# Kernel optimization log

Hardware: AMD Instinct MI355X
Metric: run time of the kernel (lower is better)

The kernel has to match this reference:

```python
import jax, jax.numpy as jnp
import numpy as np

BATCH, HORIZON = 512, 512
DIM_IN, DIM_OUT, DIM_X, DIM_NL = 64, 64, 256, 128
EPS = 1e-3  # pos_def_tol
STD = 0.5   # initialization_std


def setup_inputs() -> dict:
    key = jax.random.key(0)
    ks = jax.random.split(key, 7)
    n2 = 2 * DIM_X + DIM_NL  # 640
    return {
        "u_in": jax.random.normal(ks[0], (BATCH, HORIZON, DIM_IN), jnp.float32),
        "X":   jax.random.normal(ks[1], (n2, n2), jnp.float32) * STD,
        "Y":   jax.random.normal(ks[2], (DIM_X, DIM_X), jnp.float32) * STD,
        "B2":  jax.random.normal(ks[3], (DIM_X, DIM_IN), jnp.float32) * STD,
        "C2":  jax.random.normal(ks[4], (DIM_OUT, DIM_X), jnp.float32) * STD,
        "D21": jax.random.normal(ks[5], (DIM_OUT, DIM_NL), jnp.float32) * STD,
        "D12": jax.random.normal(ks[6], (DIM_NL, DIM_IN), jnp.float32) * STD,
    }


def _ren_run(u_in, X, Y, B2, C2, D21, D12):
    n, q = DIM_X, DIM_NL
    # Contraction-preserving matrix construction: H = X^T X + eps*I, block split.
    H = X.T @ X + EPS * jnp.eye(2 * n + q, dtype=X.dtype)
    H11 = H[:n, :n]
    H21 = H[n:n + q, :n]
    H22 = H[n:n + q, n:n + q]
    H31 = H[n + q:, :n]
    H32 = H[n + q:, n:n + q]
    H33 = H[n + q:, n + q:]
    Fm, B1 = H31, H32
    E = 0.5 * (H11 + H33 + Y - Y.T)
    E_inv = jnp.linalg.inv(E)
    Lam = 0.5 * jnp.diag(H22)          # (q,) positive diagonal of Lambda
    D11 = -jnp.tril(H22, -1)           # strictly lower triangular
    C1 = -H21

    batch, horizon = u_in.shape[0], u_in.shape[1]
    x0 = jnp.zeros((batch, n), u_in.dtype)  # x_init = 0 (defaults)

    def step(x, u_t):
        # Terms not depending on w (hoisted out of the substitution loop).
        base = x @ C1.T + u_t @ D12.T  # (B, q)

        # Forward substitution through the implicit layer: w_i = tanh(v_i / Lam_i),
        # with v_i depending only on w_{<i} since D11 is strictly lower triangular.
        def body(i, w):
            v = base[:, i] + w @ D11[i]          # (B,)
            return w.at[:, i].set(jnp.tanh(v / Lam[i]))

        w = jax.lax.fori_loop(0, q, body, jnp.zeros((batch, q), u_in.dtype))
        x_new = (x @ Fm.T + w @ B1.T + u_t @ B2.T) @ E_inv.T
        y = x_new @ C2.T + w @ D21.T
        return x_new, y

    # run(): first output is y_init (= C2 @ x_init = 0), then horizon-1 forward steps.
    u_seq = jnp.swapaxes(u_in[:, :horizon - 1, :], 0, 1)  # (T-1, B, dim_in)
    _, ys = jax.lax.scan(step, x0, u_seq)                 # (T-1, B, dim_out)
    y0 = jnp.zeros((batch, 1, DIM_OUT), u_in.dtype)
    return jnp.concatenate([y0, jnp.swapaxes(ys, 0, 1)], axis=1)


def reference(u_in, X, Y, B2, C2, D21, D12):
    return _ren_run(u_in, X, Y, B2, C2, D21, D12)
```

## Files before the change

### kernel.cpp

```cpp
#include <hip/hip_runtime.h>
#include <math.h>
#include <stddef.h>

#define NTWO 640
#define DXN 256
#define DNLN 128
#define DINN 64
#define DOUTN 64
#define BATCHN 512
#define HORN 512
#define EPSV 1.0e-3

typedef unsigned int uint;
typedef unsigned short ushort;
typedef _Float16 half2_t __attribute__((ext_vector_type(2)));

__device__ __forceinline__ float fdot2(uint a, uint b, float c) {
#if __has_builtin(__builtin_amdgcn_fdot2)
  return __builtin_amdgcn_fdot2(__builtin_bit_cast(half2_t, a),
                                __builtin_bit_cast(half2_t, b), c, false);
#else
  half2_t x = __builtin_bit_cast(half2_t, a), y = __builtin_bit_cast(half2_t, b);
  return c + (float)x[0] * (float)y[0] + (float)x[1] * (float)y[1];
#endif
}

__device__ __forceinline__ uint pack_f16(float x, float y) {
  _Float16 hx = (_Float16)x, hy = (_Float16)y;
  ushort ux = __builtin_bit_cast(ushort, hx), uy = __builtin_bit_cast(ushort, hy);
  return ((uint)uy << 16) | (uint)ux;
}

__device__ __forceinline__ float fast_exp2(float x) {
#if __has_builtin(__builtin_amdgcn_exp2f)
  return __builtin_amdgcn_exp2f(x);
#else
  return exp2f(x);
#endif
}

__device__ __forceinline__ float bcast_lane(float v, int l) {
#if __has_builtin(__builtin_amdgcn_readlane)
  return __builtin_bit_cast(float, __builtin_amdgcn_readlane(__builtin_bit_cast(int, v), l));
#else
  return __shfl(v, l, 64);
#endif
}

__device__ __forceinline__ uint comp4(const uint4& v, int k) {
  switch (k & 3) {
    case 0: return v.x;
    case 1: return v.y;
    case 2: return v.z;
    default: return v.w;
  }
}


__global__ void k_xtx(const float* __restrict__ X, double* __restrict__ H) {
  __shared__ float sA[16][17];
  __shared__ float sB[16][17];
  const int tx = threadIdx.x, ty = threadIdx.y;
  const int bi = blockIdx.y * 16, bj = blockIdx.x * 16;
  double acc = 0.0;
  for (int k0 = 0; k0 < NTWO; k0 += 16) {
    sA[ty][tx] = X[(k0 + ty) * NTWO + bi + tx];
    sB[ty][tx] = X[(k0 + ty) * NTWO + bj + tx];
    __syncthreads();
#pragma unroll
    for (int kk = 0; kk < 16; ++kk)
      acc += (double)sA[kk][ty] * (double)sB[kk][tx];
    __syncthreads();
  }
  const int i = bi + ty, j = bj + tx;
  if (i == j) acc += EPSV;
  H[i * NTWO + j] = acc;
}

__global__ void k_prep(const double* __restrict__ H, const float* __restrict__ Y,
                       const float* __restrict__ B2, const float* __restrict__ C2,
                       const float* __restrict__ D21,
                       double* __restrict__ E, double* __restrict__ scv,
                       double* __restrict__ B2d, double* __restrict__ C2d,
                       double* __restrict__ Dxt, double* __restrict__ Eye2) {
  int idx = blockIdx.x * 256 + threadIdx.x;
  if (idx < 65536) {
    int i = idx >> 8, j = idx & 255;
    E[idx] = 0.5 * (H[i * NTWO + j] + H[(384 + i) * NTWO + 384 + j]
                    + (double)Y[i * 256 + j] - (double)Y[j * 256 + i]);
    return;
  }
  idx -= 65536;
  if (idx < 128) {
    double lam = 0.5 * H[(256 + idx) * NTWO + 256 + idx];
    scv[idx] = 2.8853900817779268 / lam;
    return;
  }
  idx -= 128;
  if (idx < 16384) { B2d[idx] = (double)B2[idx]; return; }
  idx -= 16384;
  if (idx < 16384) { C2d[idx] = (double)C2[idx]; return; }
  idx -= 16384;
  if (idx < 28672) {
    int r = idx / 448, c = idx % 448;
    double v = 0.0;
    if (c >= 256 && c < 384) v = (double)D21[r * 128 + (c - 256)];
    Dxt[idx] = v;
    return;
  }
  idx -= 28672;
  if (idx < 16384) {
    int r = idx >> 7, c = idx & 127;
    Eye2[idx] = (r == c) ? 2.0 : 0.0;
  }
}

__global__ void k_ginv32(const double* __restrict__ A, int lda, float* __restrict__ Out) {
  __shared__ float M[128 * 129];
  const int tid = threadIdx.x;
  for (int i = tid; i < 128 * 128; i += 256)
    M[(i >> 7) * 129 + (i & 127)] = (float)A[(i >> 7) * lda + (i & 127)];
  __syncthreads();
  for (int k = 0; k < 128; ++k) {
    float ip = 1.0f / M[k * 129 + k];
    __syncthreads();
    if (tid < 128) {
      float v = M[k * 129 + tid];
      M[k * 129 + tid] = (tid == k) ? ip : v * ip;
    }
    __syncthreads();
    const int i0 = tid >> 1, half = tid & 1;
    float f = (i0 != k) ? M[i0 * 129 + k] : 0.0f;
    __syncthreads();
    if (i0 != k) {
      const float* rk = M + k * 129;
      float* ri = M + i0 * 129;
      const int j0 = half * 64;
#pragma unroll 8
      for (int j = j0; j < j0 + 64; ++j) {
        float v = (j == k) ? 0.0f : ri[j];
        ri[j] = v - f * rk[j];
      }
    }
    __syncthreads();
  }
  for (int i = tid; i < 128 * 128; i += 256) Out[i] = M[(i >> 7) * 129 + (i & 127)];
}

__global__ void k_dgemm(int M, int N, int K,
                        const double* __restrict__ A, int lda,
                        const double* __restrict__ B, int ldb,
                        double alpha,
                        const double* __restrict__ D, int ldd, double beta,
                        double* __restrict__ C, int ldc) {
  __shared__ double sA[16][17];
  __shared__ double sB[16][17];
  const int tx = threadIdx.x, ty = threadIdx.y;
  const int row = blockIdx.y * 16 + ty, col = blockIdx.x * 16 + tx;
  double acc = 0.0;
  for (int k0 = 0; k0 < K; k0 += 16) {
    sA[ty][tx] = A[row * lda + k0 + tx];
    sB[ty][tx] = B[(k0 + ty) * ldb + col];
    __syncthreads();
#pragma unroll
    for (int kk = 0; kk < 16; ++kk) acc += sA[ty][kk] * sB[kk][tx];
    __syncthreads();
  }
  double v = alpha * acc;
  if (beta != 0.0) v += beta * D[row * ldd + col];
  C[row * ldc + col] = v;
}

__global__ void k_copyblk(const double* __restrict__ S, int lds,
                          double* __restrict__ Dst, int ldd, int total, int cols) {
  int idx = blockIdx.x * 256 + threadIdx.x;
  if (idx < total) {
    int r = idx / cols, c = idx % cols;
    Dst[r * ldd + c] = S[r * lds + c];
  }
}

__global__ void k_cast_f2d(const float* __restrict__ s, double* __restrict__ d, int n) {
  int i = blockIdx.x * 256 + threadIdx.x;
  if (i < n) d[i] = (double)s[i];
}

__global__ void k_pack(const double* __restrict__ H, const float* __restrict__ D12,
                       const double* __restrict__ sc, const double* __restrict__ Axwu,
                       const double* __restrict__ G,
                       uint* __restrict__ Msh, uint* __restrict__ OmWh,
                       uint* __restrict__ Tp1g, uint* __restrict__ Tp2g) {
  int idx = blockIdx.x * 256 + threadIdx.x;
  if (idx < 448 * 160) {
    int rr = idx / 160, d = idx % 160;
    float v[2];
#pragma unroll
    for (int e = 0; e < 2; ++e) {
      int k = 2 * d + e;
      double x;
      if (rr < 128) {
        double s = sc[rr];
        x = (k < 256) ? (-H[(256 + rr) * NTWO + k] * s)
                      : ((double)D12[rr * DINN + (k - 256)] * s);
      } else {
        int r2 = rr - 128;
        const double* src = (r2 < 256) ? (Axwu + (size_t)r2 * 448) : (G + (size_t)(r2 - 256) * 448);
        x = (k < 256) ? src[k] : src[384 + (k - 256)];
      }
      v[e] = (float)x;
    }
    Msh[((size_t)(d >> 2) * 448 + rr) * 4 + (d & 3)] = pack_f16(v[0], v[1]);
    return;
  }
  idx -= 448 * 160;
  if (idx < 320 * 64) {
    int rr = idx / 64, d = idx % 64;
    float v[2];
#pragma unroll
    for (int e = 0; e < 2; ++e) {
      int j = 2 * d + e;
      double x = (rr < 256) ? Axwu[(size_t)rr * 448 + 256 + j]
                            : G[(size_t)(rr - 256) * 448 + 256 + j];
      v[e] = (float)x;
    }
    OmWh[((size_t)(d >> 2) * 320 + rr) * 4 + (d & 3)] = pack_f16(v[0], v[1]);
    return;
  }
  idx -= 320 * 64;
  if (idx < 4096) {
    int l = idx >> 6, d = idx & 63;
    float lo = (l > d) ? (float)(-H[(256 + l) * NTWO + 256 + d] * sc[l]) : 0.0f;
    float hi = (float)(-H[(256 + l + 64) * NTWO + 256 + d] * sc[l + 64]);
    Tp1g[idx] = pack_f16(lo, hi);
    return;
  }
  idx -= 4096;
  if (idx < 2048) {
    int l = idx >> 5, i = idx & 31;
    int j0 = 64 + 2 * i, j1 = j0 + 1;
    float v0 = (l + 64 > j0) ? (float)(-H[(256 + l + 64) * NTWO + 256 + j0] * sc[l + 64]) : 0.0f;
    float v1 = (l + 64 > j1) ? (float)(-H[(256 + l + 64) * NTWO + 256 + j1] * sc[l + 64]) : 0.0f;
    Tp2g[idx] = pack_f16(v0, v1);
  }
}

__global__ __launch_bounds__(512)
void k_scan(const float* __restrict__ u_in, const uint* __restrict__ Msh,
            const uint* __restrict__ OmWh, const uint* __restrict__ Tp1g,
            const uint* __restrict__ Tp2g, float* __restrict__ out) {
  __shared__ uint4 baseL4[40 * 128];
  __shared__ uint Tp1L[64 * 68];
  __shared__ uint Tp2L[64 * 36];
  __shared__ uint __align__(16) zL[2 * 164];
  __shared__ uint __align__(16) wvhL[2 * 64];
  const int tid = threadIdx.x;
  const int s0 = blockIdx.x * 2;
  const uint4* __restrict__ mp4 = (const uint4*)Msh;
  const uint4* __restrict__ op4 = (const uint4*)OmWh;

  for (int i = tid; i < 5120; i += 512) {
    const int blk = i >> 7, r = i & 127;
    baseL4[i] = mp4[(size_t)blk * 448 + r];
  }
  for (int i = tid; i < 4096; i += 512) Tp1L[(i >> 6) * 68 + (i & 63)] = Tp1g[i];
  for (int i = tid; i < 2048; i += 512) Tp2L[(i >> 5) * 36 + (i & 31)] = Tp2g[i];
  if (tid < 256) zL[(tid >> 7) * 164 + (tid & 127)] = 0u;
  if (tid < 128) out[((size_t)(s0 + (tid >> 6)) * HORN) * DOUTN + (tid & 63)] = 0.0f;
  if (tid >= 448) {
    const int i = tid - 448, s = i >> 5, k = i & 31;
    const float* up = u_in + ((size_t)(s0 + s) * HORN) * DINN + 2 * k;
    zL[s * 164 + 128 + k] = pack_f16(up[0], up[1]);
  }
  __syncthreads();

  for (int t = 0; t < HORN - 1; ++t) {
    float a0 = 0.f, a1 = 0.f;
    float unx = 0.f, uny = 0.f;
    uint4 om[16];
    if (tid < 128) {
      const int b = tid >> 6, l = tid & 63;
      uint4 q[16], r2[8];
      {
        const uint* tp1 = Tp1L + l * 68;
        const uint* tp2 = Tp2L + l * 36;
#pragma unroll
        for (int i = 0; i < 16; ++i) q[i] = *(const uint4*)(tp1 + 4 * i);
#pragma unroll
        for (int i = 0; i < 8; ++i) r2[i] = *(const uint4*)(tp2 + 4 * i);
      }
      const uint4* zz = (const uint4*)(zL + b * 164);
      float c0 = 0.f, c1 = 0.f;
#pragma unroll 8
      for (int i = 0; i < 40; ++i) {
        const uint4 mA = baseL4[i * 128 + l];
        const uint4 mB = baseL4[i * 128 + 64 + l];
        const uint4 p = zz[i];
        c0 = fdot2(mA.x, p.x, c0); c0 = fdot2(mA.y, p.y, c0);
        c0 = fdot2(mA.z, p.z, c0); c0 = fdot2(mA.w, p.w, c0);
        c1 = fdot2(mB.x, p.x, c1); c1 = fdot2(mB.y, p.y, c1);
        c1 = fdot2(mB.z, p.z, c1); c1 = fdot2(mB.w, p.w, c1);
      }
      __builtin_amdgcn_s_setprio(1);
      float wx = 0.f, wy = 0.f;
#pragma unroll
      for (int j = 0; j < 64; ++j) {
        const float av = bcast_lane(c0, j);
        const float sx = fast_exp2(av);
        const float rc = __builtin_amdgcn_rcpf(sx + 1.0f);
        const float w = __builtin_fmaf(-2.0f, rc, 1.0f);
        if (l == (j >> 1)) { if (j & 1) wy = w; else wx = w; }
        const half2_t h = __builtin_bit_cast(half2_t, comp4(q[j >> 2], j & 3));
        c0 = __builtin_fmaf((float)h[0], w, c0);
        c1 = __builtin_fmaf((float)h[1], w, c1);
      }
#pragma unroll
      for (int j = 64; j < 128; ++j) {
        const float av = bcast_lane(c1, j - 64);
        const float sx = fast_exp2(av);
        const float rc = __builtin_amdgcn_rcpf(sx + 1.0f);
        const float w = __builtin_fmaf(-2.0f, rc, 1.0f);
        if (l == (j >> 1)) { if (j & 1) wy = w; else wx = w; }
        const int i2 = j - 64;
        const half2_t h = __builtin_bit_cast(half2_t, comp4(r2[i2 >> 3], (i2 >> 1) & 3));
        const float tv = (i2 & 1) ? (float)h[1] : (float)h[0];
        c1 = __builtin_fmaf(tv, w, c1);
      }
      __builtin_amdgcn_s_setprio(0);
      wvhL[b * 64 + l] = pack_f16(wx, wy);
    } else if (tid < 448) {
      const int row = tid;
      const uint4* z0 = (const uint4*)zL;
      const uint4* z1 = (const uint4*)(zL + 164);
      uint4 mbuf[20];
#pragma unroll
      for (int i = 0; i < 20; ++i) mbuf[i] = mp4[(size_t)i * 448 + row];
#pragma unroll
      for (int i = 0; i < 20; ++i) {
        const uint4 m = mbuf[i];
        const uint4 p = z0[i], q = z1[i];
        a0 = fdot2(m.x, p.x, a0); a0 = fdot2(m.y, p.y, a0);
        a0 = fdot2(m.z, p.z, a0); a0 = fdot2(m.w, p.w, a0);
        a1 = fdot2(m.x, q.x, a1); a1 = fdot2(m.y, q.y, a1);
        a1 = fdot2(m.z, q.z, a1); a1 = fdot2(m.w, q.w, a1);
      }
#pragma unroll
      for (int i = 0; i < 20; ++i) mbuf[i] = mp4[(size_t)(20 + i) * 448 + row];
#pragma unroll
      for (int i = 0; i < 20; ++i) {
        const uint4 m = mbuf[i];
        const uint4 p = z0[20 + i], q = z1[20 + i];
        a0 = fdot2(m.x, p.x, a0); a0 = fdot2(m.y, p.y, a0);
        a0 = fdot2(m.z, p.z, a0); a0 = fdot2(m.w, p.w, a0);
        a1 = fdot2(m.x, q.x, a1); a1 = fdot2(m.y, q.y, a1);
        a1 = fdot2(m.z, q.z, a1); a1 = fdot2(m.w, q.w, a1);
      }
      const int rr = row - 128;
#pragma unroll
      for (int i = 0; i < 16; ++i) om[i] = op4[(size_t)i * 320 + rr];
    } else {
      const int i = tid - 448, s = i >> 5, k = i & 31;
      const float* up = u_in + ((size_t)(s0 + s) * HORN + (t + 1)) * DINN + 2 * k;
      unx = up[0]; uny = up[1];
    }
    __syncthreads();

    if (tid >= 128 && tid < 448) {
      const int row = tid;
      const uint4* wp0 = (const uint4*)wvhL;
      const uint4* wp1 = (const uint4*)(wvhL + 64);
#pragma unroll
      for (int i = 0; i < 16; ++i) {
        const uint4 m = om[i];
        const uint4 p = wp0[i], q = wp1[i];
        a0 = fdot2(m.x, p.x, a0); a0 = fdot2(m.y, p.y, a0);
        a0 = fdot2(m.z, p.z, a0); a0 = fdot2(m.w, p.w, a0);
        a1 = fdot2(m.x, q.x, a1); a1 = fdot2(m.y, q.y, a1);
        a1 = fdot2(m.z, q.z, a1); a1 = fdot2(m.w, q.w, a1);
      }
      if (row < 384) {
        const float n0 = __shfl_down(a0, 1, 64);
        const float n1 = __shfl_down(a1, 1, 64);
        if ((row & 1) == 0) {
          const int d = (row - 128) >> 1;
          zL[d] = pack_f16(a0, n0);
          zL[164 + d] = pack_f16(a1, n1);
        }
      } else {
        const int yr = row - 384;
        out[((size_t)s0 * HORN + (t + 1)) * DOUTN + yr] = a0;
        out[((size_t)(s0 + 1) * HORN + (t + 1)) * DOUTN + yr] = a1;
      }
    } else if (tid >= 448) {
      const int i = tid - 448, s = i >> 5, k = i & 31;
      zL[s * 164 + 128 + k] = pack_f16(unx, uny);
    }
    __syncthreads();
  }
}

extern "C" void kernel_launch(void* const* d_in, const int* in_sizes, int n_in,
                              void* d_out, int out_size, void* d_ws, size_t ws_size,
                              hipStream_t stream) {
  (void)in_sizes; (void)n_in; (void)out_size; (void)ws_size;
  const float* u_in = (const float*)d_in[0];
  const float* X    = (const float*)d_in[1];
  const float* Y    = (const float*)d_in[2];
  const float* B2   = (const float*)d_in[3];
  const float* C2   = (const float*)d_in[4];
  const float* D21  = (const float*)d_in[5];
  const float* D12  = (const float*)d_in[6];
  float* out = (float*)d_out;

  double* H    = (double*)d_ws;
  double* E    = H + 640 * 640;
  double* Ai   = E + 256 * 256;
  double* CMm  = Ai + 128 * 128;
  double* MBm  = CMm + 128 * 128;
  double* Sm   = MBm + 128 * 128;
  double* Tm   = Sm + 128 * 128;
  double* Einv = Tm + 128 * 128;
  double* Axwu = Einv + 256 * 256;
  double* G    = Axwu + 256 * 448;
  double* B2d  = G + 64 * 448;
  double* C2d  = B2d + 256 * 64;
  double* Dxt  = C2d + 64 * 256;
  double* Eye2 = Dxt + 64 * 448;
  double* M0d  = Eye2 + 128 * 128;
  double* Rb   = M0d + 128 * 128;
  double* scv  = Rb + 128 * 128;
  float*  F32  = (float*)(scv + 128);
  uint*   Msh  = (uint*)(F32 + 128 * 128);
  uint*   OmWh = Msh + 71680;
  uint*   Tp1g = OmWh + 20480;
  uint*   Tp2g = Tp1g + 4096;

  dim3 blk16(16, 16);
  k_xtx<<<dim3(40, 40), blk16, 0, stream>>>(X, H);
  k_prep<<<561, 256, 0, stream>>>(H, Y, B2, C2, D21, E, scv, B2d, C2d, Dxt, Eye2);

  auto inv128 = [&](const double* A, int lda, double* Out) {
    k_ginv32<<<1, 256, 0, stream>>>(A, lda, F32);
    k_cast_f2d<<<64, 256, 0, stream>>>(F32, M0d, 128 * 128);
    k_dgemm<<<dim3(8, 8), blk16, 0, stream>>>(128, 128, 128, A, lda, M0d, 128, -1.0, Eye2, 128, 1.0, Rb, 128);
    k_dgemm<<<dim3(8, 8), blk16, 0, stream>>>(128, 128, 128, M0d, 128, Rb, 128, 1.0, (const double*)nullptr, 0, 0.0, Out, 128);
  };

  const double* EA = E;
  const double* EB = E + 128;
  const double* EC = E + 128 * 256;
  const double* ED = E + 128 * 256 + 128;

  inv128(EA, 256, Ai);
  k_dgemm<<<dim3(8, 8), blk16, 0, stream>>>(128, 128, 128, EC, 256, Ai, 128, 1.0, (const double*)nullptr, 0, 0.0, CMm, 128);
  k_dgemm<<<dim3(8, 8), blk16, 0, stream>>>(128, 128, 128, Ai, 128, EB, 256, 1.0, (const double*)nullptr, 0, 0.0, MBm, 128);
  k_dgemm<<<dim3(8, 8), blk16, 0, stream>>>(128, 128, 128, CMm, 128, EB, 256, -1.0, ED, 256, 1.0, Sm, 128);
  inv128(Sm, 128, Tm);
  k_dgemm<<<dim3(8, 8), blk16, 0, stream>>>(128, 128, 128, Tm, 128, CMm, 128, -1.0, (const double*)nullptr, 0, 0.0, Einv + 128 * 256, 256);
  k_dgemm<<<dim3(8, 8), blk16, 0, stream>>>(128, 128, 128, MBm, 128, Tm, 128, -1.0, (const double*)nullptr, 0, 0.0, Einv + 128, 256);
  k_dgemm<<<dim3(8, 8), blk16, 0, stream>>>(128, 128, 128, MBm, 128, Einv + 128 * 256, 256, -1.0, Ai, 128, 1.0, Einv, 256);
  k_copyblk<<<64, 256, 0, stream>>>(Tm, 128, Einv + 128 * 256 + 128, 256, 128 * 128, 128);

  k_dgemm<<<dim3(24, 16), blk16, 0, stream>>>(256, 384, 256, Einv, 256, H + 384 * NTWO, NTWO, 1.0, (const double*)nullptr, 0, 0.0, Axwu, 448);
  k_dgemm<<<dim3(4, 16), blk16, 0, stream>>>(256, 64, 256, Einv, 256, B2d, 64, 1.0, (const double*)nullptr, 0, 0.0, Axwu + 384, 448);
  k_dgemm<<<dim3(28, 4), blk16, 0, stream>>>(64, 448, 256, C2d, 256, Axwu, 448, 1.0, Dxt, 448, 1.0, G, 448);

  k_pack<<<384, 256, 0, stream>>>(H, D12, scv, Axwu, G, Msh, OmWh, Tp1g, Tp2g);

  k_scan<<<BATCHN / 2, 512, 0, stream>>>(u_in, Msh, OmWh, Tp1g, Tp2g, out);
}
```

Measured before the change: 4.250 ms.

## Solve nonlinearity substitution two elements at a time using tanh addition identity

Rewrites the serial forward-substitution loop so each step resolves an even/odd pair of implicit-layer outputs. The odd element is computed from the even one with the tanh addition formula (tanh(a+b) = (tanh a + tanh b)/(1 + tanh a tanh b)), using a precomputed scaled coupling coefficient. Updates then use packed half2 dot products instead of two scalar FMAs. The goal is to halve the length of the serial dependency chain and the number of cross-lane broadcasts. The cost is an extra reciprocal per pair and packed fp16 rounding (round-toward-zero conversion), which may add error.

Result: slower. 4.504 ms (+6.0%).

```diff
diff --git a/kernel.cpp b/kernel.cpp
--- a/kernel.cpp
+++ b/kernel.cpp
@@ -29,6 +29,14 @@
   _Float16 hx = (_Float16)x, hy = (_Float16)y;
   ushort ux = __builtin_bit_cast(ushort, hx), uy = __builtin_bit_cast(ushort, hy);
   return ((uint)uy << 16) | (uint)ux;
+}
+
+__device__ __forceinline__ uint pack2(float x, float y) {
+#if __has_builtin(__builtin_amdgcn_cvt_pkrtz)
+  return __builtin_bit_cast(uint, __builtin_amdgcn_cvt_pkrtz(x, y));
+#else
+  return pack_f16(x, y);
+#endif
 }
 
 __device__ __forceinline__ float fast_exp2(float x) {
@@ -189,7 +197,8 @@
                        const double* __restrict__ sc, const double* __restrict__ Axwu,
                        const double* __restrict__ G,
                        uint* __restrict__ Msh, uint* __restrict__ OmWh,
-                       uint* __restrict__ Tp1g, uint* __restrict__ Tp2g) {
+                       uint* __restrict__ TAg, uint* __restrict__ TBg,
+                       uint* __restrict__ TCg, float* __restrict__ Ts2g) {
   int idx = blockIdx.x * 256 + threadIdx.x;
   if (idx < 448 * 160) {
     int rr = idx / 160, d = idx % 160;
@@ -227,30 +236,49 @@
     return;
   }
   idx -= 320 * 64;
-  if (idx < 4096) {
-    int l = idx >> 6, d = idx & 63;
-    float lo = (l > d) ? (float)(-H[(256 + l) * NTWO + 256 + d] * sc[l]) : 0.0f;
-    float hi = (float)(-H[(256 + l + 64) * NTWO + 256 + d] * sc[l + 64]);
-    Tp1g[idx] = pack_f16(lo, hi);
-    return;
-  }
-  idx -= 4096;
   if (idx < 2048) {
-    int l = idx >> 5, i = idx & 31;
-    int j0 = 64 + 2 * i, j1 = j0 + 1;
-    float v0 = (l + 64 > j0) ? (float)(-H[(256 + l + 64) * NTWO + 256 + j0] * sc[l + 64]) : 0.0f;
-    float v1 = (l + 64 > j1) ? (float)(-H[(256 + l + 64) * NTWO + 256 + j1] * sc[l + 64]) : 0.0f;
-    Tp2g[idx] = pack_f16(v0, v1);
+    int l = idx >> 5, k = idx & 31;
+    int j0 = 2 * k, j1 = 2 * k + 1;
+    float v0 = (l > j0) ? (float)(-H[(256 + l) * NTWO + 256 + j0] * sc[l]) : 0.0f;
+    float v1 = (l > j1) ? (float)(-H[(256 + l) * NTWO + 256 + j1] * sc[l]) : 0.0f;
+    TAg[idx] = pack_f16(v0, v1);
+    return;
+  }
+  idx -= 2048;
+  if (idx < 2048) {
+    int l = idx >> 5, k = idx & 31;
+    int r = l + 64;
+    float v0 = (float)(-H[(256 + r) * NTWO + 256 + 2 * k] * sc[r]);
+    float v1 = (float)(-H[(256 + r) * NTWO + 256 + 2 * k + 1] * sc[r]);
+    TBg[idx] = pack_f16(v0, v1);
+    return;
+  }
+  idx -= 2048;
+  if (idx < 2048) {
+    int l = idx >> 5, k = idx & 31;
+    int r = l + 64, j0 = 64 + 2 * k, j1 = j0 + 1;
+    float v0 = (r > j0) ? (float)(-H[(256 + r) * NTWO + 256 + j0] * sc[r]) : 0.0f;
+    float v1 = (r > j1) ? (float)(-H[(256 + r) * NTWO + 256 + j1] * sc[r]) : 0.0f;
+    TCg[idx] = pack_f16(v0, v1);
+    return;
+  }
+  idx -= 2048;
+  if (idx < 64) {
+    int k = idx;
+    Ts2g[k] = (float)(-H[(256 + 2 * k + 1) * NTWO + 256 + 2 * k] * sc[2 * k + 1]
+                      * 0.34657359027997264);
   }
 }
 
 __global__ __launch_bounds__(512)
 void k_scan(const float* __restrict__ u_in, const uint* __restrict__ Msh,
-            const uint* __restrict__ OmWh, const uint* __restrict__ Tp1g,
-            const uint* __restrict__ Tp2g, float* __restrict__ out) {
+            const uint* __restrict__ OmWh, const uint* __restrict__ TAg,
+            const uint* __restrict__ TBg, const uint* __restrict__ TCg,
+            const float* __restrict__ Ts2g, float* __restrict__ out) {
   __shared__ uint4 baseL4[40 * 128];
-  __shared__ uint Tp1L[64 * 68];
-  __shared__ uint Tp2L[64 * 36];
+  __shared__ uint TAL[64 * 36];
+  __shared__ uint TBL[64 * 36];
+  __shared__ uint TCL[64 * 36];
   __shared__ uint __align__(16) zL[2 * 164];
   __shared__ uint __align__(16) wvhL[2 * 64];
   const int tid = threadIdx.x;
@@ -262,8 +290,9 @@
     const int blk = i >> 7, r = i & 127;
     baseL4[i] = mp4[(size_t)blk * 448 + r];
   }
-  for (int i = tid; i < 4096; i += 512) Tp1L[(i >> 6) * 68 + (i & 63)] = Tp1g[i];
-  for (int i = tid; i < 2048; i += 512) Tp2L[(i >> 5) * 36 + (i & 31)] = Tp2g[i];
+  for (int i = tid; i < 2048; i += 512) TAL[(i >> 5) * 36 + (i & 31)] = TAg[i];
+  for (int i = tid; i < 2048; i += 512) TBL[(i >> 5) * 36 + (i & 31)] = TBg[i];
+  for (int i = tid; i < 2048; i += 512) TCL[(i >> 5) * 36 + (i & 31)] = TCg[i];
   if (tid < 256) zL[(tid >> 7) * 164 + (tid & 127)] = 0u;
   if (tid < 128) out[((size_t)(s0 + (tid >> 6)) * HORN) * DOUTN + (tid & 63)] = 0.0f;
   if (tid >= 448) {
@@ -271,6 +300,8 @@
     const float* up = u_in + ((size_t)(s0 + s) * HORN) * DINN + 2 * k;
     zL[s * 164 + 128 + k] = pack_f16(up[0], up[1]);
   }
+  float tsv = 0.f;
+  if (tid < 128) tsv = Ts2g[tid & 63];
   __syncthreads();
 
   for (int t = 0; t < HORN - 1; ++t) {
@@ -279,14 +310,17 @@
     uint4 om[16];
     if (tid < 128) {
       const int b = tid >> 6, l = tid & 63;
-      uint4 q[16], r2[8];
+      uint4 qa[8], qb[8], qc[8];
       {
-        const uint* tp1 = Tp1L + l * 68;
-        const uint* tp2 = Tp2L + l * 36;
-#pragma unroll
-        for (int i = 0; i < 16; ++i) q[i] = *(const uint4*)(tp1 + 4 * i);
-#pragma unroll
-        for (int i = 0; i < 8; ++i) r2[i] = *(const uint4*)(tp2 + 4 * i);
+        const uint* ta = TAL + l * 36;
+        const uint* tb = TBL + l * 36;
+        const uint* tc = TCL + l * 36;
+#pragma unroll
+        for (int i = 0; i < 8; ++i) qa[i] = *(const uint4*)(ta + 4 * i);
+#pragma unroll
+        for (int i = 0; i < 8; ++i) qb[i] = *(const uint4*)(tb + 4 * i);
+#pragma unroll
+        for (int i = 0; i < 8; ++i) qc[i] = *(const uint4*)(tc + 4 * i);
       }
       const uint4* zz = (const uint4*)(zL + b * 164);
       float c0 = 0.f, c1 = 0.f;
@@ -301,32 +335,48 @@
         c1 = fdot2(mB.z, p.z, c1); c1 = fdot2(mB.w, p.w, c1);
       }
       __builtin_amdgcn_s_setprio(1);
-      float wx = 0.f, wy = 0.f;
-#pragma unroll
-      for (int j = 0; j < 64; ++j) {
-        const float av = bcast_lane(c0, j);
-        const float sx = fast_exp2(av);
-        const float rc = __builtin_amdgcn_rcpf(sx + 1.0f);
-        const float w = __builtin_fmaf(-2.0f, rc, 1.0f);
-        if (l == (j >> 1)) { if (j & 1) wy = w; else wx = w; }
-        const half2_t h = __builtin_bit_cast(half2_t, comp4(q[j >> 2], j & 3));
-        c0 = __builtin_fmaf((float)h[0], w, c0);
-        c1 = __builtin_fmaf((float)h[1], w, c1);
-      }
-#pragma unroll
-      for (int j = 64; j < 128; ++j) {
-        const float av = bcast_lane(c1, j - 64);
-        const float sx = fast_exp2(av);
-        const float rc = __builtin_amdgcn_rcpf(sx + 1.0f);
-        const float w = __builtin_fmaf(-2.0f, rc, 1.0f);
-        if (l == (j >> 1)) { if (j & 1) wy = w; else wx = w; }
-        const int i2 = j - 64;
-        const half2_t h = __builtin_bit_cast(half2_t, comp4(r2[i2 >> 3], (i2 >> 1) & 3));
-        const float tv = (i2 & 1) ? (float)h[1] : (float)h[0];
-        c1 = __builtin_fmaf(tv, w, c1);
+      uint wcap = 0u;
+#pragma unroll
+      for (int k = 0; k < 32; ++k) {
+        const float ave = bcast_lane(c0, 2 * k);
+        const float avo = bcast_lane(c0, 2 * k + 1);
+        const float ts  = bcast_lane(tsv, k);
+        const float se = fast_exp2(ave);
+        const float so = fast_exp2(avo);
+        const float re = __builtin_amdgcn_rcpf(se + 1.0f);
+        const float ro = __builtin_amdgcn_rcpf(so + 1.0f);
+        const float we = __builtin_fmaf(-2.0f, re, 1.0f);
+        const float ws = __builtin_fmaf(-2.0f, ro, 1.0f);
+        const float tau = ts * we;
+        const float dn = __builtin_fmaf(ws, tau, 1.0f);
+        const float rd = __builtin_amdgcn_rcpf(dn);
+        const float wo = (ws + tau) * rd;
+        const uint wp = pack2(we, wo);
+        if (l == k) wcap = wp;
+        c0 = fdot2(comp4(qa[k >> 2], k & 3), wp, c0);
+        c1 = fdot2(comp4(qb[k >> 2], k & 3), wp, c1);
+      }
+#pragma unroll
+      for (int k = 32; k < 64; ++k) {
+        const float ave = bcast_lane(c1, 2 * k - 64);
+        const float avo = bcast_lane(c1, 2 * k - 63);
+        const float ts  = bcast_lane(tsv, k);
+        const float se = fast_exp2(ave);
+        const float so = fast_exp2(avo);
+        const float re = __builtin_amdgcn_rcpf(se + 1.0f);
+        const float ro = __builtin_amdgcn_rcpf(so + 1.0f);
+        const float we = __builtin_fmaf(-2.0f, re, 1.0f);
+        const float ws = __builtin_fmaf(-2.0f, ro, 1.0f);
+        const float tau = ts * we;
+        const float dn = __builtin_fmaf(ws, tau, 1.0f);
+        const float rd = __builtin_amdgcn_rcpf(dn);
+        const float wo = (ws + tau) * rd;
+        const uint wp = pack2(we, wo);
+        if (l == k) wcap = wp;
+        c1 = fdot2(comp4(qc[(k - 32) >> 2], (k - 32) & 3), wp, c1);
       }
       __builtin_amdgcn_s_setprio(0);
-      wvhL[b * 64 + l] = pack_f16(wx, wy);
+      wvhL[b * 64 + l] = wcap;
     } else if (tid < 448) {
       const int row = tid;
       const uint4* z0 = (const uint4*)zL;
@@ -431,8 +481,10 @@
   float*  F32  = (float*)(scv + 128);
   uint*   Msh  = (uint*)(F32 + 128 * 128);
   uint*   OmWh = Msh + 71680;
-  uint*   Tp1g = OmWh + 20480;
-  uint*   Tp2g = Tp1g + 4096;
+  uint*   TAg  = OmWh + 20480;
+  uint*   TBg  = TAg + 2048;
+  uint*   TCg  = TBg + 2048;
+  float*  Ts2g = (float*)(TCg + 2048);
 
   dim3 blk16(16, 16);
   k_xtx<<<dim3(40, 40), blk16, 0, stream>>>(X, H);
@@ -464,7 +516,7 @@
   k_dgemm<<<dim3(4, 16), blk16, 0, stream>>>(256, 64, 256, Einv, 256, B2d, 64, 1.0, (const double*)nullptr, 0, 0.0, Axwu + 384, 448);
   k_dgemm<<<dim3(28, 4), blk16, 0, stream>>>(64, 448, 256, C2d, 256, Axwu, 448, 1.0, Dxt, 448, 1.0, G, 448);
 
-  k_pack<<<384, 256, 0, stream>>>(H, D12, scv, Axwu, G, Msh, OmWh, Tp1g, Tp2g);
-
-  k_scan<<<BATCHN / 2, 512, 0, stream>>>(u_in, Msh, OmWh, Tp1g, Tp2g, out);
-}
+  k_pack<<<385, 256, 0, stream>>>(H, D12, scv, Axwu, G, Msh, OmWh, TAg, TBg, TCg, Ts2g);
+
+  k_scan<<<BATCHN / 2, 512, 0, stream>>>(u_in, Msh, OmWh, TAg, TBg, TCg, Ts2g, out);
+}
```
